# Performance work log

Hardware: AMD Instinct MI355X
Metric: run time of the kernel (lower is better)

Reference implementation:

```python
import jax, jax.numpy as jnp
import numpy as np

THETA = 10000.0

def apply_rope(x, positions):
    # x: [B, H, S, d_k], positions: [S] int
    d_k = x.shape[-1]
    inv_freq = THETA ** (-jnp.arange(0, d_k, 2, dtype=jnp.float32) / d_k)  # [d_k/2]
    ang = positions.astype(jnp.float32)[:, None] * inv_freq[None, :]        # [S, d_k/2]
    cos, sin = jnp.cos(ang), jnp.sin(ang)
    x_even = x[..., 0::2]
    x_odd = x[..., 1::2]
    r_even = x_even * cos - x_odd * sin
    r_odd = x_even * sin + x_odd * cos
    # interleave back
    return jnp.stack([r_even, r_odd], axis=-1).reshape(x.shape)

def setup_inputs() -> dict:
    key = jax.random.key(0)
    k1, k2, k3 = jax.random.split(key, 3)
    B, S, D = 2, 2048, 1024
    x = jax.random.normal(k1, (B, S, D), dtype=jnp.float32)
    token_positions = jnp.arange(S, dtype=jnp.int32)
    W_qkv = jax.random.normal(k2, (3 * D, D), dtype=jnp.float32) * 0.02
    W_o = jax.random.normal(k3, (D, D), dtype=jnp.float32) * 0.02
    return {"x": x, "token_positions": token_positions, "W_qkv": W_qkv, "W_o": W_o}

def reference(x, token_positions, W_qkv, W_o):
    B, S, D = x.shape
    H = 16
    d_k = D // H
    qkv = jnp.einsum('bsd,ed->bse', x, W_qkv)           # [B, S, 3D]
    q, k, v = jnp.split(qkv, 3, axis=-1)
    def to_heads(t):
        return t.reshape(B, S, H, d_k).transpose(0, 2, 1, 3)  # [B, H, S, d_k]
    hq, hk, hv = to_heads(q), to_heads(k), to_heads(v)
    hq = apply_rope(hq, token_positions)
    hk = apply_rope(hk, token_positions)
    scale = d_k ** -0.5
    scores = jnp.einsum('bhqd,bhkd->bhqk', hq, hk) * scale  # [B, H, S, S]
    causal = jnp.tril(jnp.ones((S, S), dtype=bool))
    scores = jnp.where(causal, scores, -jnp.inf)
    attn = jax.nn.softmax(scores, axis=-1)
    out = jnp.einsum('bhqk,bhkd->bhqd', attn, hv)           # [B, H, S, d_k]
    out = out.transpose(0, 2, 1, 3).reshape(B, S, D)
    return jnp.einsum('bsd,ed->bse', out, W_o)
```

## Files before the change

kernel.cpp:

```cpp
#include <hip/hip_runtime.h>
#include <math.h>

typedef short short8 __attribute__((ext_vector_type(8)));
typedef float f32x4 __attribute__((ext_vector_type(4)));

typedef __attribute__((address_space(1))) const void* as1p;
typedef __attribute__((address_space(3))) void* as3p;

__device__ __forceinline__ unsigned short f2bf(float f) {
    unsigned int u = __float_as_uint(f);
    u += 0x7fffu + ((u >> 16) & 1u);
    return (unsigned short)(u >> 16);
}
__device__ __forceinline__ float bf2f(unsigned int bits) {
    return __uint_as_float(bits << 16);
}

__global__ void cvt_all_bf16(const float* __restrict__ x,
                             const float* __restrict__ wqkv,
                             const float* __restrict__ wo,
                             unsigned short* __restrict__ xb,
                             unsigned short* __restrict__ wqkvb,
                             unsigned short* __restrict__ wob) {
    int i = blockIdx.x * blockDim.x + threadIdx.x;
    const float* src;
    unsigned short* dst;
    int off;
    if (i < 1048576)       { src = x;    dst = xb;    off = i; }
    else if (i < 1835008)  { src = wqkv; dst = wqkvb; off = i - 1048576; }
    else                   { src = wo;   dst = wob;   off = i - 1835008; }
    float4 v = ((const float4*)src)[off];
    ushort4 o = make_ushort4(f2bf(v.x), f2bf(v.y), f2bf(v.z), f2bf(v.w));
    ((ushort4*)dst)[off] = o;
}

template <int RF, bool BF16_OUT, bool DO_ROPE>
__global__ __launch_bounds__(256) void gemm_nt_mfma(
    const unsigned short* __restrict__ A, const unsigned short* __restrict__ B,
    void* __restrict__ Cv, const int* __restrict__ pos, int N, int K) {
    constexpr int BM = RF * 32;
    __shared__ unsigned short As[BM * 32];
    __shared__ unsigned short Bs[128 * 32];
    const int tid = threadIdx.x;
    const int wave = tid >> 6, lane = tid & 63;
    const int m0 = blockIdx.y * BM, n0 = blockIdx.x << 7;
    const int wr = ((wave >> 1) & 1) * (RF * 16);
    const int wc = (wave & 1) << 6;

    const int r0 = tid >> 2, ko = (tid & 3) << 3;
    const unsigned short* Ap0 = A + (size_t)(m0 + r0) * K + ko;
    const unsigned short* Ap1 = A + (size_t)(m0 + (RF == 4 ? 64 : 0) + r0) * K + ko;
    const unsigned short* Bp0 = B + (size_t)(n0 + r0) * K + ko;
    const unsigned short* Bp1 = B + (size_t)(n0 + 64 + r0) * K + ko;

    f32x4 acc[RF][4] = {};
    const int lro = lane & 15, g8 = (lane >> 4) << 3;

    for (int k0 = 0; k0 < K; k0 += 32) {
        __syncthreads();
        __builtin_amdgcn_global_load_lds((as1p)(Ap0 + k0), (as3p)(As + tid * 8), 16, 0, 0);
        if constexpr (RF == 4)
            __builtin_amdgcn_global_load_lds((as1p)(Ap1 + k0), (as3p)(As + (256 + tid) * 8), 16, 0, 0);
        __builtin_amdgcn_global_load_lds((as1p)(Bp0 + k0), (as3p)(Bs + tid * 8), 16, 0, 0);
        __builtin_amdgcn_global_load_lds((as1p)(Bp1 + k0), (as3p)(Bs + (256 + tid) * 8), 16, 0, 0);
        __syncthreads();

        short8 af[RF], bfr[4];
        #pragma unroll
        for (int i = 0; i < RF; i++) af[i] = *(const short8*)&As[(wr + i * 16 + lro) * 32 + g8];
        #pragma unroll
        for (int j = 0; j < 4; j++) bfr[j] = *(const short8*)&Bs[(wc + j * 16 + lro) * 32 + g8];
        #pragma unroll
        for (int i = 0; i < RF; i++)
            #pragma unroll
            for (int j = 0; j < 4; j++)
                acc[i][j] = __builtin_amdgcn_mfma_f32_16x16x32_bf16(af[i], bfr[j], acc[i][j], 0, 0, 0);
    }

    const int row_b = m0 + wr + ((lane >> 4) << 2);
    const int col_b = n0 + wc + lro;

    if constexpr (DO_ROPE) {
        const int sec = (n0 + wc) >> 10;
        if (sec < 2) {
            const float qs = (sec == 0) ? 0.18033688011112042f : 1.0f;
            const float sgn = (lane & 1) ? 1.0f : -1.0f;
            float ps[RF * 4];
            #pragma unroll
            for (int i = 0; i < RF; i++)
                #pragma unroll
                for (int r = 0; r < 4; r++)
                    ps[i * 4 + r] = (float)pos[(row_b + i * 16 + r) & 2047];
            #pragma unroll
            for (int j = 0; j < 4; j++) {
                float invf_rev = exp2f(-(float)((lro >> 1) + 8 * j) * 0.41524101186092029f)
                                 * 0.15915494309189535f;
                #pragma unroll
                for (int i = 0; i < RF; i++)
                    #pragma unroll
                    for (int r = 0; r < 4; r++) {
                        float rev = ps[i * 4 + r] * invf_rev;
                        rev -= floorf(rev);
                        float c = __builtin_amdgcn_cosf(rev) * qs;
                        float s = __builtin_amdgcn_sinf(rev) * (qs * sgn);
                        float mine = acc[i][j][r];
                        float partner = __shfl_xor(mine, 1, 64);
                        acc[i][j][r] = mine * c + partner * s;
                    }
            }
        }
    }

    #pragma unroll
    for (int i = 0; i < RF; i++)
        #pragma unroll
        for (int j = 0; j < 4; j++)
            #pragma unroll
            for (int r = 0; r < 4; r++) {
                size_t idx = (size_t)(row_b + i * 16 + r) * N + (col_b + j * 16);
                if constexpr (BF16_OUT) ((unsigned short*)Cv)[idx] = f2bf(acc[i][j][r]);
                else ((float*)Cv)[idx] = acc[i][j][r];
            }
}

__global__ __launch_bounds__(256) void flash_attn_mfma(
    const unsigned short* __restrict__ qkv, unsigned short* __restrict__ Ows) {
    const int S = 2048, D3 = 3072;
    const int L = blockIdx.x + (blockIdx.y << 4) + (blockIdx.z << 8);
    const int xcd = L & 7, t = L >> 3;
    const int pp = t & 15;
    const int g2 = xcd + ((t >> 4) << 3);
    const int h = g2 & 15, b = g2 >> 4;
    const int tid = threadIdx.x, wave = tid >> 6, lane = tid & 63;
    const int lro = lane & 15, grp = lane >> 4;

    __shared__ __align__(16) unsigned short Qs[64 * 64];
    __shared__ __align__(16) unsigned short Ks[2][64 * 64];
    __shared__ __align__(16) unsigned int   Vp[2][64 * 36];
    __shared__ __align__(16) unsigned short Ps[64 * 80];

    const int sr = tid >> 3;
    const int sc = ((tid & 7) ^ (sr & 7)) << 3;
    const int kp = tid >> 3, vo = (tid & 7) << 3;
    const int vka = (kp >> 1) + ((kp & 1) << 5);
    const int vcol = (((kp >> 2) ^ (tid & 7)) << 2) | (kp & 3);

    const int cq = grp ^ (lro & 7);
    int kof0[4], kof1[4], vbse[4], vq[4];
    #pragma unroll
    for (int nt = 0; nt < 4; nt++) {
        int R = nt * 16 + lro;
        kof0[nt] = R * 64 + cq * 8;
        kof1[nt] = R * 64 + (cq ^ 4) * 8;
        vbse[nt] = R * 36;
        vq[nt] = (grp ^ (R >> 3)) << 2;
    }
    const int aq0o = (wave * 16 + lro) * 64 + cq * 8;
    const int aq1o = (wave * 16 + lro) * 64 + (cq ^ 4) * 8;
    const int apo = (wave * 16 + lro) * 80 + grp * 8;
    const int prow = wave * 16 + grp * 4;

    const unsigned short* kbg = qkv + (size_t)(b * S) * D3 + 1024 + h * 64;
    const unsigned short* vbg = qkv + (size_t)(b * S) * D3 + 2048 + h * 64;

    for (int ph = 0; ph < 2; ph++) {
        const int qt = ph ? 31 - pp : pp;
        const int q0 = qt << 6;
        const int nkt = qt + 1;

        __syncthreads();
        {
            const unsigned short* qs0 = qkv + (size_t)(b * S + q0 + sr) * D3 + h * 64 + sc;
            *(uint4*)&Qs[tid * 8] = *(const uint4*)qs0;
            *(uint4*)&Qs[(tid + 256) * 8] = *(const uint4*)(qs0 + (size_t)32 * D3);
        }
        __builtin_amdgcn_global_load_lds((as1p)(kbg + (size_t)sr * D3 + sc),
                                         (as3p)&Ks[0][tid * 8], 16, 0, 0);
        __builtin_amdgcn_global_load_lds((as1p)(kbg + (size_t)(sr + 32) * D3 + sc),
                                         (as3p)&Ks[0][(tid + 256) * 8], 16, 0, 0);
        {
            const unsigned short* vs = vbg + (size_t)vka * D3 + vo;
            uint4 va = *(const uint4*)vs;
            uint4 vb = *(const uint4*)(vs + (size_t)16 * D3);
            const unsigned short* pa = (const unsigned short*)&va;
            const unsigned short* pb = (const unsigned short*)&vb;
            #pragma unroll
            for (int j = 0; j < 8; j++)
                Vp[0][(vo + j) * 36 + vcol] = (unsigned)pa[j] | ((unsigned)pb[j] << 16);
        }
        __syncthreads();

        f32x4 acc_o[4] = {};
        float lsum[4] = {0.f, 0.f, 0.f, 0.f};
        short8 aq0 = *(const short8*)&Qs[aq0o];
        short8 aq1 = *(const short8*)&Qs[aq1o];

        for (int kt = 0; kt < nkt; kt++) {
            const int cur = kt & 1, nxt = cur ^ 1;
            const bool pf = (kt + 1 < nkt);
            uint4 va, vb;
            if (pf) {
                const unsigned short* kb1 = kbg + (size_t)((kt + 1) * 64) * D3;
                __builtin_amdgcn_global_load_lds((as1p)(kb1 + (size_t)sr * D3 + sc),
                                                 (as3p)&Ks[nxt][tid * 8], 16, 0, 0);
                __builtin_amdgcn_global_load_lds((as1p)(kb1 + (size_t)(sr + 32) * D3 + sc),
                                                 (as3p)&Ks[nxt][(tid + 256) * 8], 16, 0, 0);
                const unsigned short* vs = vbg + (size_t)((kt + 1) * 64 + vka) * D3 + vo;
                va = *(const uint4*)vs;
                vb = *(const uint4*)(vs + (size_t)16 * D3);
            }

            f32x4 s[4] = {};
            #pragma unroll
            for (int nt = 0; nt < 4; nt++) {
                short8 bk0 = *(const short8*)&Ks[cur][kof0[nt]];
                short8 bk1 = *(const short8*)&Ks[cur][kof1[nt]];
                s[nt] = __builtin_amdgcn_mfma_f32_16x16x32_bf16(aq0, bk0, s[nt], 0, 0, 0);
                s[nt] = __builtin_amdgcn_mfma_f32_16x16x32_bf16(aq1, bk1, s[nt], 0, 0, 0);
            }

            const bool diag = (kt == nkt - 1);
            #pragma unroll
            for (int r = 0; r < 4; r++) {
                float v0 = s[0][r], v1 = s[1][r], v2 = s[2][r], v3 = s[3][r];
                if (diag) {
                    int rowl = prow + r;
                    if (lro > rowl) v0 = -1e30f;
                    if (16 + lro > rowl) v1 = -1e30f;
                    if (32 + lro > rowl) v2 = -1e30f;
                    if (48 + lro > rowl) v3 = -1e30f;
                }
                float p0 = __builtin_amdgcn_exp2f(v0);
                float p1 = __builtin_amdgcn_exp2f(v1);
                float p2 = __builtin_amdgcn_exp2f(v2);
                float p3 = __builtin_amdgcn_exp2f(v3);
                lsum[r] += (p0 + p1) + (p2 + p3);
                unsigned u0 = __float_as_uint(p0) + 0x8000u;
                unsigned u1 = __float_as_uint(p1) + 0x8000u;
                unsigned u2 = __float_as_uint(p2) + 0x8000u;
                unsigned u3 = __float_as_uint(p3) + 0x8000u;
                uint2 w = make_uint2((u0 >> 16) | (u1 & 0xffff0000u),
                                     (u2 >> 16) | (u3 & 0xffff0000u));
                *(uint2*)&Ps[(prow + r) * 80 + lro * 4] = w;
            }

            short8 ap0 = *(const short8*)&Ps[apo];
            short8 ap1 = *(const short8*)&Ps[apo + 32];
            #pragma unroll
            for (int nt = 0; nt < 4; nt++) {
                short8 bv0 = *(const short8*)&Vp[cur][vbse[nt] + vq[nt]];
                short8 bv1 = *(const short8*)&Vp[cur][vbse[nt] + (vq[nt] ^ 16)];
                acc_o[nt] = __builtin_amdgcn_mfma_f32_16x16x32_bf16(ap0, bv0, acc_o[nt], 0, 0, 0);
                acc_o[nt] = __builtin_amdgcn_mfma_f32_16x16x32_bf16(ap1, bv1, acc_o[nt], 0, 0, 0);
            }

            if (pf) {
                const unsigned short* pa = (const unsigned short*)&va;
                const unsigned short* pb = (const unsigned short*)&vb;
                #pragma unroll
                for (int j = 0; j < 8; j++)
                    Vp[nxt][(vo + j) * 36 + vcol] = (unsigned)pa[j] | ((unsigned)pb[j] << 16);
            }
            __syncthreads();
        }

        #pragma unroll
        for (int r = 0; r < 4; r++) {
            float rsum = lsum[r];
            #pragma unroll
            for (int off = 1; off < 16; off <<= 1)
                rsum += __shfl_xor(rsum, off, 16);
            float inv = 1.0f / rsum;
            int row = q0 + prow + r;
            #pragma unroll
            for (int nt = 0; nt < 4; nt++)
                Ows[(size_t)(b * S + row) * 1024 + h * 64 + nt * 16 + lro] =
                    f2bf(acc_o[nt][r] * inv);
        }
    }
}

extern "C" void kernel_launch(void* const* d_in, const int* in_sizes, int n_in,
                              void* d_out, int out_size, void* d_ws, size_t ws_size,
                              hipStream_t stream) {
    const float* x    = (const float*)d_in[0];
    const int*   pos  = (const int*)d_in[1];
    const float* Wqkv = (const float*)d_in[2];
    const float* Wo   = (const float*)d_in[3];
    float* out = (float*)d_out;

    unsigned short* xb    = (unsigned short*)d_ws;
    unsigned short* Wqkvb = xb + (size_t)4096 * 1024;
    unsigned short* Wob   = Wqkvb + (size_t)3072 * 1024;
    unsigned short* qkvb  = Wob + (size_t)1024 * 1024;
    unsigned short* Owsb  = qkvb + (size_t)4096 * 3072;

    cvt_all_bf16<<<8192, 256, 0, stream>>>(x, Wqkv, Wo, xb, Wqkvb, Wob);

    gemm_nt_mfma<4, true, true><<<dim3(24, 32), 256, 0, stream>>>(
        xb, Wqkvb, qkvb, pos, 3072, 1024);

    flash_attn_mfma<<<dim3(16, 16, 2), 256, 0, stream>>>(qkvb, Owsb);

    gemm_nt_mfma<2, false, false><<<dim3(8, 64), 256, 0, stream>>>(
        Owsb, Wob, out, nullptr, 1024, 1024);
}
```

Baseline: 186.5 us.

## Split attention into one q-tile per block and remap GEMM blocks per XCD

Result: slower. 201.2 us (+7.9%).

```diff
diff --git a/kernel.cpp b/kernel.cpp
--- a/kernel.cpp
+++ b/kernel.cpp
@@ -34,7 +34,7 @@
     ((ushort4*)dst)[off] = o;
 }
 
-template <int RF, bool BF16_OUT, bool DO_ROPE>
+template <int RF, int NTX, bool BF16_OUT, bool DO_ROPE>
 __global__ __launch_bounds__(256) void gemm_nt_mfma(
     const unsigned short* __restrict__ A, const unsigned short* __restrict__ B,
     void* __restrict__ Cv, const int* __restrict__ pos, int N, int K) {
@@ -43,7 +43,11 @@
     __shared__ unsigned short Bs[128 * 32];
     const int tid = threadIdx.x;
     const int wave = tid >> 6, lane = tid & 63;
-    const int m0 = blockIdx.y * BM, n0 = blockIdx.x << 7;
+    const int L = blockIdx.x;
+    const int xcd = L & 7, idx = L >> 3;
+    const int nt_ = xcd * NTX + idx % NTX;
+    const int mt  = idx / NTX;
+    const int m0 = mt * BM, n0 = nt_ << 7;
     const int wr = ((wave >> 1) & 1) * (RF * 16);
     const int wc = (wave & 1) << 6;
 
@@ -117,24 +121,24 @@
         for (int j = 0; j < 4; j++)
             #pragma unroll
             for (int r = 0; r < 4; r++) {
-                size_t idx = (size_t)(row_b + i * 16 + r) * N + (col_b + j * 16);
-                if constexpr (BF16_OUT) ((unsigned short*)Cv)[idx] = f2bf(acc[i][j][r]);
-                else ((float*)Cv)[idx] = acc[i][j][r];
+                size_t idx2 = (size_t)(row_b + i * 16 + r) * N + (col_b + j * 16);
+                if constexpr (BF16_OUT) ((unsigned short*)Cv)[idx2] = f2bf(acc[i][j][r]);
+                else ((float*)Cv)[idx2] = acc[i][j][r];
             }
 }
 
 __global__ __launch_bounds__(256) void flash_attn_mfma(
     const unsigned short* __restrict__ qkv, unsigned short* __restrict__ Ows) {
     const int S = 2048, D3 = 3072;
-    const int L = blockIdx.x + (blockIdx.y << 4) + (blockIdx.z << 8);
+    const int L = blockIdx.x;
     const int xcd = L & 7, t = L >> 3;
-    const int pp = t & 15;
-    const int g2 = xcd + ((t >> 4) << 3);
+    const int g2 = xcd + ((t >> 5) << 3);
     const int h = g2 & 15, b = g2 >> 4;
+    const int qt = 31 - (t & 31);
+    const int q0 = qt << 6, nkt = qt + 1;
     const int tid = threadIdx.x, wave = tid >> 6, lane = tid & 63;
     const int lro = lane & 15, grp = lane >> 4;
 
-    __shared__ __align__(16) unsigned short Qs[64 * 64];
     __shared__ __align__(16) unsigned short Ks[2][64 * 64];
     __shared__ __align__(16) unsigned int   Vp[2][64 * 36];
     __shared__ __align__(16) unsigned short Ps[64 * 80];
@@ -155,128 +159,117 @@
         vbse[nt] = R * 36;
         vq[nt] = (grp ^ (R >> 3)) << 2;
     }
-    const int aq0o = (wave * 16 + lro) * 64 + cq * 8;
-    const int aq1o = (wave * 16 + lro) * 64 + (cq ^ 4) * 8;
     const int apo = (wave * 16 + lro) * 80 + grp * 8;
     const int prow = wave * 16 + grp * 4;
 
     const unsigned short* kbg = qkv + (size_t)(b * S) * D3 + 1024 + h * 64;
     const unsigned short* vbg = qkv + (size_t)(b * S) * D3 + 2048 + h * 64;
 
-    for (int ph = 0; ph < 2; ph++) {
-        const int qt = ph ? 31 - pp : pp;
-        const int q0 = qt << 6;
-        const int nkt = qt + 1;
-
-        __syncthreads();
-        {
-            const unsigned short* qs0 = qkv + (size_t)(b * S + q0 + sr) * D3 + h * 64 + sc;
-            *(uint4*)&Qs[tid * 8] = *(const uint4*)qs0;
-            *(uint4*)&Qs[(tid + 256) * 8] = *(const uint4*)(qs0 + (size_t)32 * D3);
-        }
-        __builtin_amdgcn_global_load_lds((as1p)(kbg + (size_t)sr * D3 + sc),
-                                         (as3p)&Ks[0][tid * 8], 16, 0, 0);
-        __builtin_amdgcn_global_load_lds((as1p)(kbg + (size_t)(sr + 32) * D3 + sc),
-                                         (as3p)&Ks[0][(tid + 256) * 8], 16, 0, 0);
-        {
-            const unsigned short* vs = vbg + (size_t)vka * D3 + vo;
-            uint4 va = *(const uint4*)vs;
-            uint4 vb = *(const uint4*)(vs + (size_t)16 * D3);
+    const unsigned short* qrow =
+        qkv + (size_t)(b * S + q0 + wave * 16 + lro) * D3 + h * 64 + grp * 8;
+    short8 aq0 = *(const short8*)qrow;
+    short8 aq1 = *(const short8*)(qrow + 32);
+
+    __builtin_amdgcn_global_load_lds((as1p)(kbg + (size_t)sr * D3 + sc),
+                                     (as3p)&Ks[0][tid * 8], 16, 0, 0);
+    __builtin_amdgcn_global_load_lds((as1p)(kbg + (size_t)(sr + 32) * D3 + sc),
+                                     (as3p)&Ks[0][(tid + 256) * 8], 16, 0, 0);
+    {
+        const unsigned short* vs = vbg + (size_t)vka * D3 + vo;
+        uint4 va = *(const uint4*)vs;
+        uint4 vb = *(const uint4*)(vs + (size_t)16 * D3);
+        const unsigned short* pa = (const unsigned short*)&va;
+        const unsigned short* pb = (const unsigned short*)&vb;
+        #pragma unroll
+        for (int j = 0; j < 8; j++)
+            Vp[0][(vo + j) * 36 + vcol] = (unsigned)pa[j] | ((unsigned)pb[j] << 16);
+    }
+    __syncthreads();
+
+    f32x4 acc_o[4] = {};
+    float lsum[4] = {0.f, 0.f, 0.f, 0.f};
+
+    for (int kt = 0; kt < nkt; kt++) {
+        const int cur = kt & 1, nxt = cur ^ 1;
+        const bool pf = (kt + 1 < nkt);
+        uint4 va, vb;
+        if (pf) {
+            const unsigned short* kb1 = kbg + (size_t)((kt + 1) * 64) * D3;
+            __builtin_amdgcn_global_load_lds((as1p)(kb1 + (size_t)sr * D3 + sc),
+                                             (as3p)&Ks[nxt][tid * 8], 16, 0, 0);
+            __builtin_amdgcn_global_load_lds((as1p)(kb1 + (size_t)(sr + 32) * D3 + sc),
+                                             (as3p)&Ks[nxt][(tid + 256) * 8], 16, 0, 0);
+            const unsigned short* vs = vbg + (size_t)((kt + 1) * 64 + vka) * D3 + vo;
+            va = *(const uint4*)vs;
+            vb = *(const uint4*)(vs + (size_t)16 * D3);
+        }
+
+        f32x4 s[4] = {};
+        #pragma unroll
+        for (int nt = 0; nt < 4; nt++) {
+            short8 bk0 = *(const short8*)&Ks[cur][kof0[nt]];
+            short8 bk1 = *(const short8*)&Ks[cur][kof1[nt]];
+            s[nt] = __builtin_amdgcn_mfma_f32_16x16x32_bf16(aq0, bk0, s[nt], 0, 0, 0);
+            s[nt] = __builtin_amdgcn_mfma_f32_16x16x32_bf16(aq1, bk1, s[nt], 0, 0, 0);
+        }
+
+        const bool diag = (kt == nkt - 1);
+        #pragma unroll
+        for (int r = 0; r < 4; r++) {
+            float v0 = s[0][r], v1 = s[1][r], v2 = s[2][r], v3 = s[3][r];
+            if (diag) {
+                int rowl = prow + r;
+                if (lro > rowl) v0 = -1e30f;
+                if (16 + lro > rowl) v1 = -1e30f;
+                if (32 + lro > rowl) v2 = -1e30f;
+                if (48 + lro > rowl) v3 = -1e30f;
+            }
+            float p0 = __builtin_amdgcn_exp2f(v0);
+            float p1 = __builtin_amdgcn_exp2f(v1);
+            float p2 = __builtin_amdgcn_exp2f(v2);
+            float p3 = __builtin_amdgcn_exp2f(v3);
+            lsum[r] += (p0 + p1) + (p2 + p3);
+            unsigned u0 = __float_as_uint(p0) + 0x8000u;
+            unsigned u1 = __float_as_uint(p1) + 0x8000u;
+            unsigned u2 = __float_as_uint(p2) + 0x8000u;
+            unsigned u3 = __float_as_uint(p3) + 0x8000u;
+            uint2 w = make_uint2((u0 >> 16) | (u1 & 0xffff0000u),
+                                 (u2 >> 16) | (u3 & 0xffff0000u));
+            *(uint2*)&Ps[(prow + r) * 80 + lro * 4] = w;
+        }
+
+        short8 ap0 = *(const short8*)&Ps[apo];
+        short8 ap1 = *(const short8*)&Ps[apo + 32];
+        #pragma unroll
+        for (int nt = 0; nt < 4; nt++) {
+            short8 bv0 = *(const short8*)&Vp[cur][vbse[nt] + vq[nt]];
+            short8 bv1 = *(const short8*)&Vp[cur][vbse[nt] + (vq[nt] ^ 16)];
+            acc_o[nt] = __builtin_amdgcn_mfma_f32_16x16x32_bf16(ap0, bv0, acc_o[nt], 0, 0, 0);
+            acc_o[nt] = __builtin_amdgcn_mfma_f32_16x16x32_bf16(ap1, bv1, acc_o[nt], 0, 0, 0);
+        }
+
+        if (pf) {
             const unsigned short* pa = (const unsigned short*)&va;
             const unsigned short* pb = (const unsigned short*)&vb;
             #pragma unroll
             for (int j = 0; j < 8; j++)
-                Vp[0][(vo + j) * 36 + vcol] = (unsigned)pa[j] | ((unsigned)pb[j] << 16);
+                Vp[nxt][(vo + j) * 36 + vcol] = (unsigned)pa[j] | ((unsigned)pb[j] << 16);
         }
         __syncthreads();
-
-        f32x4 acc_o[4] = {};
-        float lsum[4] = {0.f, 0.f, 0.f, 0.f};
-        short8 aq0 = *(const short8*)&Qs[aq0o];
-        short8 aq1 = *(const short8*)&Qs[aq1o];
-
-        for (int kt = 0; kt < nkt; kt++) {
-            const int cur = kt & 1, nxt = cur ^ 1;
-            const bool pf = (kt + 1 < nkt);
-            uint4 va, vb;
-            if (pf) {
-                const unsigned short* kb1 = kbg + (size_t)((kt + 1) * 64) * D3;
-                __builtin_amdgcn_global_load_lds((as1p)(kb1 + (size_t)sr * D3 + sc),
-                                                 (as3p)&Ks[nxt][tid * 8], 16, 0, 0);
-                __builtin_amdgcn_global_load_lds((as1p)(kb1 + (size_t)(sr + 32) * D3 + sc),
-                                                 (as3p)&Ks[nxt][(tid + 256) * 8], 16, 0, 0);
-                const unsigned short* vs = vbg + (size_t)((kt + 1) * 64 + vka) * D3 + vo;
-                va = *(const uint4*)vs;
-                vb = *(const uint4*)(vs + (size_t)16 * D3);
-            }
-
-            f32x4 s[4] = {};
-            #pragma unroll
-            for (int nt = 0; nt < 4; nt++) {
-                short8 bk0 = *(const short8*)&Ks[cur][kof0[nt]];
-                short8 bk1 = *(const short8*)&Ks[cur][kof1[nt]];
-                s[nt] = __builtin_amdgcn_mfma_f32_16x16x32_bf16(aq0, bk0, s[nt], 0, 0, 0);
-                s[nt] = __builtin_amdgcn_mfma_f32_16x16x32_bf16(aq1, bk1, s[nt], 0, 0, 0);
-            }
-
-            const bool diag = (kt == nkt - 1);
-            #pragma unroll
-            for (int r = 0; r < 4; r++) {
-                float v0 = s[0][r], v1 = s[1][r], v2 = s[2][r], v3 = s[3][r];
-                if (diag) {
-                    int rowl = prow + r;
-                    if (lro > rowl) v0 = -1e30f;
-                    if (16 + lro > rowl) v1 = -1e30f;
-                    if (32 + lro > rowl) v2 = -1e30f;
-                    if (48 + lro > rowl) v3 = -1e30f;
-                }
-                float p0 = __builtin_amdgcn_exp2f(v0);
-                float p1 = __builtin_amdgcn_exp2f(v1);
-                float p2 = __builtin_amdgcn_exp2f(v2);
-                float p3 = __builtin_amdgcn_exp2f(v3);
-                lsum[r] += (p0 + p1) + (p2 + p3);
-                unsigned u0 = __float_as_uint(p0) + 0x8000u;
-                unsigned u1 = __float_as_uint(p1) + 0x8000u;
-                unsigned u2 = __float_as_uint(p2) + 0x8000u;
-                unsigned u3 = __float_as_uint(p3) + 0x8000u;
-                uint2 w = make_uint2((u0 >> 16) | (u1 & 0xffff0000u),
-                                     (u2 >> 16) | (u3 & 0xffff0000u));
-                *(uint2*)&Ps[(prow + r) * 80 + lro * 4] = w;
-            }
-
-            short8 ap0 = *(const short8*)&Ps[apo];
-            short8 ap1 = *(const short8*)&Ps[apo + 32];
-            #pragma unroll
-            for (int nt = 0; nt < 4; nt++) {
-                short8 bv0 = *(const short8*)&Vp[cur][vbse[nt] + vq[nt]];
-                short8 bv1 = *(const short8*)&Vp[cur][vbse[nt] + (vq[nt] ^ 16)];
-                acc_o[nt] = __builtin_amdgcn_mfma_f32_16x16x32_bf16(ap0, bv0, acc_o[nt], 0, 0, 0);
-                acc_o[nt] = __builtin_amdgcn_mfma_f32_16x16x32_bf16(ap1, bv1, acc_o[nt], 0, 0, 0);
-            }
-
-            if (pf) {
-                const unsigned short* pa = (const unsigned short*)&va;
-                const unsigned short* pb = (const unsigned short*)&vb;
-                #pragma unroll
-                for (int j = 0; j < 8; j++)
-                    Vp[nxt][(vo + j) * 36 + vcol] = (unsigned)pa[j] | ((unsigned)pb[j] << 16);
-            }
-            __syncthreads();
-        }
-
-        #pragma unroll
-        for (int r = 0; r < 4; r++) {
-            float rsum = lsum[r];
-            #pragma unroll
-            for (int off = 1; off < 16; off <<= 1)
-                rsum += __shfl_xor(rsum, off, 16);
-            float inv = 1.0f / rsum;
-            int row = q0 + prow + r;
-            #pragma unroll
-            for (int nt = 0; nt < 4; nt++)
-                Ows[(size_t)(b * S + row) * 1024 + h * 64 + nt * 16 + lro] =
-                    f2bf(acc_o[nt][r] * inv);
-        }
+    }
+
+    #pragma unroll
+    for (int r = 0; r < 4; r++) {
+        float rsum = lsum[r];
+        #pragma unroll
+        for (int off = 1; off < 16; off <<= 1)
+            rsum += __shfl_xor(rsum, off, 16);
+        float inv = 1.0f / rsum;
+        int row = q0 + prow + r;
+        #pragma unroll
+        for (int nt = 0; nt < 4; nt++)
+            Ows[(size_t)(b * S + row) * 1024 + h * 64 + nt * 16 + lro] =
+                f2bf(acc_o[nt][r] * inv);
     }
 }
 
@@ -297,11 +290,11 @@
 
     cvt_all_bf16<<<8192, 256, 0, stream>>>(x, Wqkv, Wo, xb, Wqkvb, Wob);
 
-    gemm_nt_mfma<4, true, true><<<dim3(24, 32), 256, 0, stream>>>(
+    gemm_nt_mfma<4, 3, true, true><<<768, 256, 0, stream>>>(
         xb, Wqkvb, qkvb, pos, 3072, 1024);
 
-    flash_attn_mfma<<<dim3(16, 16, 2), 256, 0, stream>>>(qkvb, Owsb);
-
-    gemm_nt_mfma<2, false, false><<<dim3(8, 64), 256, 0, stream>>>(
+    flash_attn_mfma<<<1024, 256, 0, stream>>>(qkvb, Owsb);
+
+    gemm_nt_mfma<2, 1, false, false><<<512, 256, 0, stream>>>(
         Owsb, Wob, out, nullptr, 1024, 1024);
 }
```
